# Kernel tuning notes

Measured on AMD Instinct MI355X. Metric: run time of the kernel, lower is better.

The kernel has to match this reference:

```python
import jax, jax.numpy as jnp
import numpy as np

NEG_SLOPE = 0.2


def gat_layer(x, src, dst, W, a_src, a_dst, b, heads, out_c, concat):
    N = x.shape[0]
    h = (x @ W).reshape(N, heads, out_c)                      # [N,H,C]
    alpha_s = jnp.einsum('nhc,hc->nh', h, a_src)              # [N,H]
    alpha_d = jnp.einsum('nhc,hc->nh', h, a_dst)              # [N,H]
    e = jax.nn.leaky_relu(alpha_s[src] + alpha_d[dst], NEG_SLOPE)  # [E,H]
    # softmax over incoming edges per destination node (segment softmax)
    m = jax.ops.segment_max(e, dst, num_segments=N)
    m = jnp.where(jnp.isfinite(m), m, 0.0)
    ex = jnp.exp(e - m[dst])
    denom = jax.ops.segment_sum(ex, dst, num_segments=N)
    alpha = ex / (denom[dst] + 1e-16)                         # [E,H]
    out = jax.ops.segment_sum(alpha[:, :, None] * h[src], dst, num_segments=N)  # [N,H,C]
    out = out.reshape(N, heads * out_c) if concat else out.mean(axis=1)
    return out + b


def setup_inputs() -> dict:
    key = jax.random.key(0)
    ks = jax.random.split(key, 12)
    N, E, D, H, C, G = 20000, 160000, 256, 4, 128, 64
    x = jax.random.normal(ks[0], (N, D), dtype=jnp.float32)
    edge_index = jax.random.randint(ks[1], (2, E), 0, N)
    batch = jnp.sort(jax.random.randint(ks[2], (N,), 0, G))
    s = 0.05
    params = {
        'W1': jax.random.normal(ks[3], (D, H * C), jnp.float32) * s,
        'a_src1': jax.random.normal(ks[4], (H, C), jnp.float32) * s,
        'a_dst1': jax.random.normal(ks[5], (H, C), jnp.float32) * s,
        'b1': jnp.zeros((H * C,), jnp.float32),
        'W2': jax.random.normal(ks[6], (H * C, C), jnp.float32) * s,
        'a_src2': jax.random.normal(ks[7], (1, C), jnp.float32) * s,
        'a_dst2': jax.random.normal(ks[8], (1, C), jnp.float32) * s,
        'b2': jnp.zeros((C,), jnp.float32),
        'fc1_W': jax.random.normal(ks[9], (C, C // 2), jnp.float32) * s,
        'fc1_b': jnp.zeros((C // 2,), jnp.float32),
        'fc2_W': jax.random.normal(ks[10], (C // 2, 1), jnp.float32) * s,
        'fc2_b': jnp.zeros((1,), jnp.float32),
    }
    return dict(x=x, edge_index=edge_index, batch=batch, **params)


def reference(x, edge_index, batch, W1, a_src1, a_dst1, b1, W2, a_src2, a_dst2, b2,
              fc1_W, fc1_b, fc2_W, fc2_b):
    N = x.shape[0]
    G = 64  # number of graphs
    # add self-loops (PyG GATConv default)
    loop = jnp.arange(N, dtype=edge_index.dtype)
    src = jnp.concatenate([edge_index[0], loop])
    dst = jnp.concatenate([edge_index[1], loop])
    h = jax.nn.relu(gat_layer(x, src, dst, W1, a_src1, a_dst1, b1, 4, 128, True))
    h = gat_layer(h, src, dst, W2, a_src2, a_dst2, b2, 1, 128, False)
    # global mean pool per graph
    sums = jax.ops.segment_sum(h, batch, num_segments=G)
    cnts = jax.ops.segment_sum(jnp.ones((N,), h.dtype), batch, num_segments=G)
    pooled = sums / jnp.maximum(cnts, 1.0)[:, None]          # [G,128]
    out = jax.nn.relu(pooled @ fc1_W + fc1_b)
    return out @ fc2_W + fc2_b                                # [G,1]
```

## Files before the change

### kernel.cpp

```cpp
#include <hip/hip_runtime.h>
#include <hip/hip_bf16.h>
#include <cstdint>
#include <cstddef>

#define NEG_SLOPE 0.2f

typedef __attribute__((ext_vector_type(8))) __bf16 bf16x8;
typedef __attribute__((ext_vector_type(4))) __bf16 bf16x4;
typedef __attribute__((ext_vector_type(2))) __bf16 bf16x2;
typedef __attribute__((ext_vector_type(4))) float  f32x4;

__device__ __forceinline__ float lrelu(float v) {
    return (v < 0.f) ? NEG_SLOPE * v : v;
}

__device__ __forceinline__ unsigned fkey(float x) {
    unsigned b = __float_as_uint(x);
    return b ^ (unsigned)(((int)b >> 31) | 0x80000000);
}
__device__ __forceinline__ float funkey(unsigned k) {
    unsigned b = (k & 0x80000000u) ? (k ^ 0x80000000u) : ~k;
    return __uint_as_float(b);
}

__global__ __launch_bounds__(256) void gemm2_sum(
    const __bf16* __restrict__ A,
    const __bf16* __restrict__ Bt,
    __bf16* __restrict__ Cout,
    const float* __restrict__ ps_part, const float* __restrict__ pd_part,
    float* __restrict__ as2, float* __restrict__ ad2,
    unsigned* __restrict__ gmax2u,
    int M, int MB)
{
    if ((int)blockIdx.y >= MB) {
        int chunk = ((int)blockIdx.y - MB) * 2 + (int)blockIdx.x;
        int i = chunk * 256 + threadIdx.x;
        float lm = -1e30f;
        if (i < M) {
            float4 p = *(const float4*)&ps_part[(size_t)i * 4];
            float4 q = *(const float4*)&pd_part[(size_t)i * 4];
            float s = (p.x + p.y) + (p.z + p.w);
            float d = (q.x + q.y) + (q.z + q.w);
            as2[i] = s;
            ad2[i] = d;
            lm = s;
        }
        #pragma unroll
        for (int t = 1; t < 64; t <<= 1) lm = fmaxf(lm, __shfl_xor(lm, t));
        if ((threadIdx.x & 63) == 0) atomicMax(gmax2u, fkey(lm));
        return;
    }

    const int tid  = threadIdx.x;
    const int wave = tid >> 6, lane = tid & 63;
    const int wr = wave >> 1, wc = wave & 1;
    const int rowbase = blockIdx.y * 64 + wr * 32;
    const int colbase = blockIdx.x * 64 + wc * 32;
    const int l15 = lane & 15, kg = lane >> 4;
    const int K = 512, N = 128;

    size_t aoff[2], boff[2];
    #pragma unroll
    for (int mf = 0; mf < 2; ++mf) {
        int r = rowbase + mf * 16 + l15;
        if (r > M - 1) r = M - 1;
        aoff[mf] = (size_t)r * K + kg * 8;
    }
    #pragma unroll
    for (int nf = 0; nf < 2; ++nf) {
        int c = colbase + nf * 16 + l15;
        boff[nf] = (size_t)c * K + kg * 8;
    }

    f32x4 acc[2][2];
    #pragma unroll
    for (int mf = 0; mf < 2; ++mf)
        #pragma unroll
        for (int nf = 0; nf < 2; ++nf)
            acc[mf][nf] = (f32x4){0.f, 0.f, 0.f, 0.f};

    #pragma unroll 2
    for (int k0 = 0; k0 < K; k0 += 32) {
        bf16x8 af[2], bfr[2];
        #pragma unroll
        for (int mf = 0; mf < 2; ++mf)
            af[mf] = *(const bf16x8*)(A + aoff[mf] + k0);
        #pragma unroll
        for (int nf = 0; nf < 2; ++nf)
            bfr[nf] = *(const bf16x8*)(Bt + boff[nf] + k0);
        #pragma unroll
        for (int mf = 0; mf < 2; ++mf)
            #pragma unroll
            for (int nf = 0; nf < 2; ++nf)
                acc[mf][nf] = __builtin_amdgcn_mfma_f32_16x16x32_bf16(af[mf], bfr[nf], acc[mf][nf], 0, 0, 0);
    }

    #pragma unroll
    for (int mf = 0; mf < 2; ++mf)
        #pragma unroll
        for (int j = 0; j < 4; ++j) {
            int r = rowbase + mf * 16 + kg * 4 + j;
            if (r < M) {
                #pragma unroll
                for (int nf = 0; nf < 2; ++nf) {
                    int c = colbase + nf * 16 + l15;
                    Cout[(size_t)r * N + c] = (__bf16)acc[mf][nf][j];
                }
            }
        }
}

__global__ __launch_bounds__(256) void gemm1_agg(
    const __bf16* __restrict__ aggx,
    const __bf16* __restrict__ w1t,
    const float* __restrict__ b1, const float* __restrict__ wsd2,
    __bf16* __restrict__ out1b,
    float* __restrict__ ps_part, float* __restrict__ pd_part,
    int M)
{
    const int head = blockIdx.x;
    const int tid  = threadIdx.x;
    const int wave = tid >> 6, lane = tid & 63;
    const int wr = wave >> 1, wc = wave & 1;
    const int rowbase = blockIdx.y * 128 + wr * 64;
    const int l15 = lane & 15, kg = lane >> 4;

    size_t aoff[4], boff[4];
    #pragma unroll
    for (int mf = 0; mf < 4; ++mf) {
        int r = rowbase + mf * 16 + l15;
        if (r > M - 1) r = M - 1;
        aoff[mf] = (size_t)r * 1024 + head * 256 + kg * 8;
    }
    #pragma unroll
    for (int nf = 0; nf < 4; ++nf) {
        int c = head * 128 + wc * 64 + nf * 16 + l15;
        boff[nf] = (size_t)c * 256 + kg * 8;
    }

    f32x4 acc[4][4];
    #pragma unroll
    for (int mf = 0; mf < 4; ++mf)
        #pragma unroll
        for (int nf = 0; nf < 4; ++nf)
            acc[mf][nf] = (f32x4){0.f, 0.f, 0.f, 0.f};

    #pragma unroll 2
    for (int k0 = 0; k0 < 256; k0 += 32) {
        bf16x8 af[4], bfr[4];
        #pragma unroll
        for (int mf = 0; mf < 4; ++mf)
            af[mf] = *(const bf16x8*)(aggx + aoff[mf] + k0);
        #pragma unroll
        for (int nf = 0; nf < 4; ++nf)
            bfr[nf] = *(const bf16x8*)(w1t + boff[nf] + k0);
        #pragma unroll
        for (int mf = 0; mf < 4; ++mf)
            #pragma unroll
            for (int nf = 0; nf < 4; ++nf)
                acc[mf][nf] = __builtin_amdgcn_mfma_f32_16x16x32_bf16(af[mf], bfr[nf], acc[mf][nf], 0, 0, 0);
    }

    __shared__ float smp[2][128], smd[2][128];

    #pragma unroll
    for (int mf = 0; mf < 4; ++mf)
        #pragma unroll
        for (int j = 0; j < 4; ++j) {
            int r = rowbase + mf * 16 + kg * 4 + j;
            float ps = 0.f, pd = 0.f;
            #pragma unroll
            for (int nf = 0; nf < 4; ++nf) {
                int col = head * 128 + wc * 64 + nf * 16 + l15;
                float o = fmaxf(acc[mf][nf][j] + b1[col], 0.f);
                if (r < M)
                    out1b[(size_t)r * 512 + col] = (__bf16)o;
                ps = fmaf(o, wsd2[col], ps);
                pd = fmaf(o, wsd2[512 + col], pd);
            }
            #pragma unroll
            for (int t = 1; t < 16; t <<= 1) {
                ps += __shfl_xor(ps, t);
                pd += __shfl_xor(pd, t);
            }
            if (l15 == 0) {
                int lr = wr * 64 + mf * 16 + kg * 4 + j;
                smp[wc][lr] = ps;
                smd[wc][lr] = pd;
            }
        }
    __syncthreads();
    if (tid < 128) {
        int r = blockIdx.y * 128 + tid;
        if (r < M) {
            ps_part[(size_t)r * 4 + head] = smp[0][tid] + smp[1][tid];
            pd_part[(size_t)r * 4 + head] = smd[0][tid] + smd[1][tid];
        }
    }
}

__global__ void prep_kernel(const float* __restrict__ W1, const float* __restrict__ W2,
                            const float* __restrict__ as1w, const float* __restrict__ ad1w,
                            const float* __restrict__ as2w, const float* __restrict__ ad2w,
                            const int* __restrict__ batch,
                            __bf16* __restrict__ w1t, __bf16* __restrict__ w2t,
                            float* __restrict__ wsd1, float* __restrict__ wsd2,
                            int* __restrict__ gstart, int* __restrict__ cnt,
                            unsigned* __restrict__ gmax2u,
                            int N, int G)
{
    int t = blockIdx.x * 256 + threadIdx.x;
    if (t < 131072) {
        int i = t;
        int k = i >> 9, n = i & 511;
        w1t[n * 256 + k] = (__bf16)W1[i];
    } else if (t < 196608) {
        int j = t - 131072;
        int k = j >> 7, n = j & 127;
        w2t[n * 512 + k] = (__bf16)W2[j];
    } else if (t < 199680) {
        int t2 = t - 196608;
        if (t2 < 2048) {
            int k = t2 >> 3, v = t2 & 7, h = v >> 1;
            const float* av = (v & 1) ? (ad1w + h * 128) : (as1w + h * 128);
            float s = 0.f;
            for (int c = 0; c < 128; ++c) s += W1[k * 512 + h * 128 + c] * av[c];
            wsd1[v * 256 + k] = s;
        } else {
            int t3 = t2 - 2048;
            int k = t3 >> 1, v = t3 & 1;
            const float* av = v ? ad2w : as2w;
            float s = 0.f;
            for (int c = 0; c < 128; ++c) s += W2[k * 128 + c] * av[c];
            wsd2[v * 512 + k] = s;
        }
    } else if (t < 199680 + N) {
        int n = t - 199680;
        int b    = batch[n];
        int prev = (n == 0) ? -1 : batch[n - 1];
        for (int g = prev + 1; g <= b; ++g) gstart[g] = n;
        if (n == N - 1) {
            for (int g = b + 1; g <= G; ++g) gstart[g] = N;
        }
    } else if (t < 199680 + 2 * N) {
        cnt[t - 199680 - N] = 0;
    } else if (t == 199680 + 2 * N) {
        *gmax2u = fkey(-1e30f);
    }
}

__global__ __launch_bounds__(256) void count_cvtx(
    const int* __restrict__ ei, int* __restrict__ cnt,
    const float* __restrict__ x, const float* __restrict__ wsd1,
    __bf16* __restrict__ xb, float* __restrict__ as1_, float* __restrict__ ad1_,
    int ET, int E0, int N, int CB)
{
    if ((int)blockIdx.x < CB) {
        int base = (blockIdx.x * 256 + threadIdx.x) * 2;
        #pragma unroll
        for (int k = 0; k < 2; ++k) {
            int e = base + k;
            if (e < ET) {
                int d = (e < E0) ? ei[E0 + e] : (e - E0);
                atomicAdd(&cnt[d], 1);
            }
        }
        return;
    }
    int bid = blockIdx.x - CB;
    int wave = threadIdx.x >> 6, lane = threadIdx.x & 63;
    int n = bid * 4 + wave;
    if (n >= N) return;
    float4 xv = *(const float4*)&x[(size_t)n * 256 + lane * 4];
    bf16x4 xo;
    xo[0] = (__bf16)xv.x; xo[1] = (__bf16)xv.y; xo[2] = (__bf16)xv.z; xo[3] = (__bf16)xv.w;
    *(bf16x4*)&xb[(size_t)n * 256 + lane * 4] = xo;
    float p[8];
    #pragma unroll
    for (int v = 0; v < 8; ++v) {
        float4 wv = *(const float4*)&wsd1[v * 256 + lane * 4];
        p[v] = xv.x * wv.x + xv.y * wv.y + xv.z * wv.z + xv.w * wv.w;
    }
    #pragma unroll
    for (int v = 0; v < 8; ++v)
        #pragma unroll
        for (int s = 1; s < 64; s <<= 1) p[v] += __shfl_xor(p[v], s);
    if (lane == 0) {
        #pragma unroll
        for (int h = 0; h < 4; ++h) {
            as1_[n * 4 + h] = p[2 * h];
            ad1_[n * 4 + h] = p[2 * h + 1];
        }
    }
}

__global__ __launch_bounds__(1024) void scan_gmax(
    const int* __restrict__ cnt, int* __restrict__ offs, int* __restrict__ cur,
    const float* __restrict__ as1_, float* __restrict__ gmax1, int n)
{
    constexpr int CHUNK = 20;
    int t = threadIdx.x;
    int base = t * CHUNK;
    int v[CHUNK];
    int s = 0;
    #pragma unroll
    for (int i = 0; i < CHUNK; ++i) {
        int idx = base + i;
        int xv = (idx < n) ? cnt[idx] : 0;
        v[i] = s; s += xv;
    }
    int lane = t & 63, w = t >> 6;
    int sc = s;
    #pragma unroll
    for (int d = 1; d < 64; d <<= 1) {
        int o = __shfl_up(sc, d);
        if (lane >= d) sc += o;
    }
    __shared__ int wt[16], wb[17];
    __shared__ float gsm[16][4];
    if (lane == 63) wt[w] = sc;
    __syncthreads();
    if (t == 0) {
        int acc = 0;
        for (int i = 0; i < 16; ++i) { wb[i] = acc; acc += wt[i]; }
        wb[16] = acc;
    }
    __syncthreads();
    int ebase = wb[w] + (sc - s);
    #pragma unroll
    for (int i = 0; i < CHUNK; ++i) {
        int idx = base + i;
        if (idx < n) {
            int o = ebase + v[i];
            offs[idx] = o;
            cur[idx]  = o;
        }
    }
    if (t == 0) offs[n] = wb[16];

    float lm0 = -1e30f, lm1 = -1e30f, lm2 = -1e30f, lm3 = -1e30f;
    for (int i = t; i < n; i += 1024) {
        float4 a = *(const float4*)&as1_[(size_t)i * 4];
        lm0 = fmaxf(lm0, a.x); lm1 = fmaxf(lm1, a.y);
        lm2 = fmaxf(lm2, a.z); lm3 = fmaxf(lm3, a.w);
    }
    #pragma unroll
    for (int d = 1; d < 64; d <<= 1) {
        lm0 = fmaxf(lm0, __shfl_xor(lm0, d));
        lm1 = fmaxf(lm1, __shfl_xor(lm1, d));
        lm2 = fmaxf(lm2, __shfl_xor(lm2, d));
        lm3 = fmaxf(lm3, __shfl_xor(lm3, d));
    }
    if (lane == 0) {
        gsm[w][0] = lm0; gsm[w][1] = lm1; gsm[w][2] = lm2; gsm[w][3] = lm3;
    }
    __syncthreads();
    if (t == 0) {
        float m0 = -1e30f, m1 = -1e30f, m2 = -1e30f, m3 = -1e30f;
        for (int i = 0; i < 16; ++i) {
            m0 = fmaxf(m0, gsm[i][0]); m1 = fmaxf(m1, gsm[i][1]);
            m2 = fmaxf(m2, gsm[i][2]); m3 = fmaxf(m3, gsm[i][3]);
        }
        gmax1[0] = m0; gmax1[1] = m1; gmax1[2] = m2; gmax1[3] = m3;
    }
}

__global__ void scatter_kernel(const int* __restrict__ ei, int* __restrict__ cur,
                               int* __restrict__ srcs, int ET, int E0)
{
    int e = blockIdx.x * blockDim.x + threadIdx.x;
    if (e >= ET) return;
    int d = (e < E0) ? ei[E0 + e] : (e - E0);
    int s = (e < E0) ? ei[e] : (e - E0);
    int pos = atomicAdd(&cur[d], 1);
    srcs[pos] = s;
}

__global__ __launch_bounds__(256) void aggx_kernel(
    const __bf16* __restrict__ xb, const int* __restrict__ offs,
    const int* __restrict__ srcs,
    const float* __restrict__ as1_, const float* __restrict__ ad1_,
    const float* __restrict__ gmax1,
    __bf16* __restrict__ aggx, int N)
{
    __shared__ float w4s[4][64][4];
    __shared__ int   sidx[4][64];
    int wave = threadIdx.x >> 6, lane = threadIdx.x & 63;
    int n = blockIdx.x * 4 + wave;
    if (n >= N) return;
    int s0 = offs[n], s1 = offs[n + 1];
    float4 adv = *(const float4*)&ad1_[(size_t)n * 4];
    float m0 = lrelu(gmax1[0] + adv.x);
    float m1 = lrelu(gmax1[1] + adv.y);
    float m2 = lrelu(gmax1[2] + adv.z);
    float m3 = lrelu(gmax1[3] + adv.w);

    float d0 = 0.f, d1 = 0.f, d2 = 0.f, d3 = 0.f;
    float a0[4] = {0.f,0.f,0.f,0.f}, a1[4] = {0.f,0.f,0.f,0.f};
    float a2[4] = {0.f,0.f,0.f,0.f}, a3[4] = {0.f,0.f,0.f,0.f};
    const __bf16* xbase = xb + lane * 4;

    for (int base = s0; base < s1; base += 64) {
        int cnt = min(64, s1 - base);
        if (lane < cnt) {
            int s = srcs[base + lane];
            float4 av = *(const float4*)&as1_[(size_t)s * 4];
            float w0 = __expf(lrelu(av.x + adv.x) - m0);
            float w1 = __expf(lrelu(av.y + adv.y) - m1);
            float w2 = __expf(lrelu(av.z + adv.z) - m2);
            float w3 = __expf(lrelu(av.w + adv.w) - m3);
            d0 += w0; d1 += w1; d2 += w2; d3 += w3;
            sidx[wave][lane] = s;
            w4s[wave][lane][0] = w0; w4s[wave][lane][1] = w1;
            w4s[wave][lane][2] = w2; w4s[wave][lane][3] = w3;
        }
        int j = 0;
        for (; j + 7 < cnt; j += 8) {
            int s_[8]; float4 w_[8]; bf16x4 xv_[8];
            #pragma unroll
            for (int i = 0; i < 8; ++i) {
                s_[i] = sidx[wave][j + i];
                w_[i] = *(const float4*)&w4s[wave][j + i][0];
            }
            #pragma unroll
            for (int i = 0; i < 8; ++i)
                xv_[i] = *(const bf16x4*)(xbase + (size_t)s_[i] * 256);
            #pragma unroll
            for (int i = 0; i < 8; ++i) {
                float xf[4];
                #pragma unroll
                for (int c = 0; c < 4; ++c) xf[c] = (float)xv_[i][c];
                #pragma unroll
                for (int c = 0; c < 4; ++c) {
                    a0[c] = fmaf(w_[i].x, xf[c], a0[c]);
                    a1[c] = fmaf(w_[i].y, xf[c], a1[c]);
                    a2[c] = fmaf(w_[i].z, xf[c], a2[c]);
                    a3[c] = fmaf(w_[i].w, xf[c], a3[c]);
                }
            }
        }
        for (; j < cnt; ++j) {
            int s = sidx[wave][j];
            float4 w = *(const float4*)&w4s[wave][j][0];
            bf16x4 xv = *(const bf16x4*)(xbase + (size_t)s * 256);
            float xf[4];
            #pragma unroll
            for (int c = 0; c < 4; ++c) xf[c] = (float)xv[c];
            #pragma unroll
            for (int c = 0; c < 4; ++c) {
                a0[c] = fmaf(w.x, xf[c], a0[c]);
                a1[c] = fmaf(w.y, xf[c], a1[c]);
                a2[c] = fmaf(w.z, xf[c], a2[c]);
                a3[c] = fmaf(w.w, xf[c], a3[c]);
            }
        }
    }

    #pragma unroll
    for (int t = 1; t < 64; t <<= 1) {
        d0 += __shfl_xor(d0, t);
        d1 += __shfl_xor(d1, t);
        d2 += __shfl_xor(d2, t);
        d3 += __shfl_xor(d3, t);
    }

    float i0 = 1.f / (d0 + 1e-16f);
    float i1 = 1.f / (d1 + 1e-16f);
    float i2 = 1.f / (d2 + 1e-16f);
    float i3 = 1.f / (d3 + 1e-16f);
    __bf16* obase = aggx + (size_t)n * 1024 + lane * 4;
    bf16x4 o;
    #pragma unroll
    for (int c = 0; c < 4; ++c) o[c] = (__bf16)(a0[c] * i0);
    *(bf16x4*)(obase + 0)   = o;
    #pragma unroll
    for (int c = 0; c < 4; ++c) o[c] = (__bf16)(a1[c] * i1);
    *(bf16x4*)(obase + 256) = o;
    #pragma unroll
    for (int c = 0; c < 4; ++c) o[c] = (__bf16)(a2[c] * i2);
    *(bf16x4*)(obase + 512) = o;
    #pragma unroll
    for (int c = 0; c < 4; ++c) o[c] = (__bf16)(a3[c] * i3);
    *(bf16x4*)(obase + 768) = o;
}

__global__ __launch_bounds__(256) void aggregate2_kernel(
    const __bf16* __restrict__ h2b, const int* __restrict__ offs,
    const int* __restrict__ srcs,
    const float* __restrict__ as2, const float* __restrict__ ad2,
    const unsigned* __restrict__ gmax2u,
    const float* __restrict__ b2, float* __restrict__ out2, int N)
{
    __shared__ float wls[4][64];
    __shared__ int   sidx[4][64];
    int wave = threadIdx.x >> 6, lane = threadIdx.x & 63;
    int n = blockIdx.x * 4 + wave;
    if (n >= N) return;
    int s0 = offs[n], s1 = offs[n + 1];
    float adn = ad2[n];
    float m = lrelu(funkey(*gmax2u) + adn);

    float den = 0.f;
    float c0 = 0.f, c1 = 0.f;
    const __bf16* hbase = h2b + lane * 2;

    for (int base = s0; base < s1; base += 64) {
        int cnt = min(64, s1 - base);
        if (lane < cnt) {
            int s = srcs[base + lane];
            float w = __expf(lrelu(as2[s] + adn) - m);
            den += w;
            sidx[wave][lane] = s;
            wls[wave][lane]  = w;
        }
        int j = 0;
        for (; j + 7 < cnt; j += 8) {
            int s_[8]; float w_[8]; bf16x2 h_[8];
            #pragma unroll
            for (int i = 0; i < 8; ++i) {
                s_[i] = sidx[wave][j + i];
                w_[i] = wls[wave][j + i];
            }
            #pragma unroll
            for (int i = 0; i < 8; ++i)
                h_[i] = *(const bf16x2*)(hbase + (size_t)s_[i] * 128);
            #pragma unroll
            for (int i = 0; i < 8; ++i) {
                c0 = fmaf(w_[i], (float)h_[i][0], c0);
                c1 = fmaf(w_[i], (float)h_[i][1], c1);
            }
        }
        for (; j < cnt; ++j) {
            int s = sidx[wave][j];
            float w = wls[wave][j];
            bf16x2 hv = *(const bf16x2*)(hbase + (size_t)s * 128);
            c0 = fmaf(w, (float)hv[0], c0);
            c1 = fmaf(w, (float)hv[1], c1);
        }
    }

    #pragma unroll
    for (int t = 1; t < 64; t <<= 1) den += __shfl_xor(den, t);
    float inv = 1.f / (den + 1e-16f);
    float2 o;
    o.x = c0 * inv + b2[lane * 2 + 0];
    o.y = c1 * inv + b2[lane * 2 + 1];
    *(float2*)&out2[(size_t)n * 128 + lane * 2] = o;
}

#define POOL_S 16
__global__ void pool_stage1(const float* __restrict__ out2, const int* __restrict__ gstart,
                            float* __restrict__ partial, int C)
{
    int g = blockIdx.x, slice = blockIdx.y;
    int c = threadIdx.x;
    int s = gstart[g], e = gstart[g + 1];
    int len = e - s;
    int chunk = (len + POOL_S - 1) / POOL_S;
    int n0 = s + slice * chunk;
    int n1 = min(n0 + chunk, e);
    float acc = 0.f;
    for (int n = n0; n < n1; ++n) acc += out2[(size_t)n * C + c];
    partial[((size_t)g * POOL_S + slice) * C + c] = acc;
}

__global__ __launch_bounds__(128) void pool_head(
    const float* __restrict__ partial, const int* __restrict__ gstart,
    const float* __restrict__ fc1W, const float* __restrict__ fc1b,
    const float* __restrict__ fc2W, const float* __restrict__ fc2b,
    float* __restrict__ out)
{
    int g = blockIdx.x;
    int t = threadIdx.x;
    __shared__ float pl[128];
    float acc = 0.f;
    #pragma unroll
    for (int s = 0; s < POOL_S; ++s)
        acc += partial[((size_t)g * POOL_S + s) * 128 + t];
    float cntf = (float)(gstart[g + 1] - gstart[g]);
    pl[t] = acc / fmaxf(cntf, 1.0f);
    __syncthreads();
    if (t < 64) {
        float v = 0.f;
        for (int c = 0; c < 128; ++c)
            v += pl[c] * fc1W[c * 64 + t];
        v = fmaxf(v + fc1b[t], 0.f) * fc2W[t];
        #pragma unroll
        for (int s = 32; s > 0; s >>= 1) v += __shfl_down(v, s);
        if (t == 0) out[g] = v + fc2b[0];
    }
}

extern "C" void kernel_launch(void* const* d_in, const int* in_sizes, int n_in,
                              void* d_out, int out_size, void* d_ws, size_t ws_size,
                              hipStream_t stream)
{
    const float* x    = (const float*)d_in[0];
    const int*   ei   = (const int*)d_in[1];
    const int*   batch= (const int*)d_in[2];
    const float* W1   = (const float*)d_in[3];
    const float* as1w = (const float*)d_in[4];
    const float* ad1w = (const float*)d_in[5];
    const float* b1   = (const float*)d_in[6];
    const float* W2   = (const float*)d_in[7];
    const float* as2w = (const float*)d_in[8];
    const float* ad2w = (const float*)d_in[9];
    const float* b2   = (const float*)d_in[10];
    const float* fc1W = (const float*)d_in[11];
    const float* fc1b = (const float*)d_in[12];
    const float* fc2W = (const float*)d_in[13];
    const float* fc2b = (const float*)d_in[14];
    float* out = (float*)d_out;

    const int D = 256, C = 128, G = 64;
    const int N  = in_sizes[0] / D;
    const int E0 = in_sizes[1] / 2;
    const int ET = E0 + N;

    char* p = (char*)d_ws;
    auto alloc = [&](size_t bytes) -> char* {
        char* r = p;
        p += (bytes + 255) & ~(size_t)255;
        return r;
    };
    __bf16* xb    = (__bf16*)alloc((size_t)N * D * 2);
    __bf16* aggx  = (__bf16*)alloc((size_t)N * 4 * 256 * 2);
    __bf16* out1b = (__bf16*)alloc((size_t)N * 512 * 2);
    __bf16* h2b   = (__bf16*)alloc((size_t)N * C * 2);
    float*  out2  = (float*)alloc((size_t)N * C * 4);
    __bf16* w1t   = (__bf16*)alloc((size_t)256 * 512 * 2);
    __bf16* w2t   = (__bf16*)alloc((size_t)512 * 128 * 2);
    float* wsd1   = (float*)alloc(8 * 256 * 4);
    float* wsd2   = (float*)alloc(2 * 512 * 4);
    float* gmax1  = (float*)alloc(4 * 4);
    unsigned* gmax2u = (unsigned*)alloc(4);
    float* as1_   = (float*)alloc((size_t)N * 4 * 4);
    float* ad1_   = (float*)alloc((size_t)N * 4 * 4);
    float* ps_part= (float*)alloc((size_t)N * 4 * 4);
    float* pd_part= (float*)alloc((size_t)N * 4 * 4);
    float* as2    = (float*)alloc((size_t)N * 4);
    float* ad2    = (float*)alloc((size_t)N * 4);
    int*   cnt    = (int*)alloc((size_t)N * 4);
    int*   cur    = (int*)alloc((size_t)N * 4);
    int*   offs   = (int*)alloc((size_t)(N + 1) * 4);
    int*   srcs   = (int*)alloc((size_t)ET * 4);
    int*   gstart = (int*)alloc((size_t)(G + 1) * 4);
    float* partial= (float*)alloc((size_t)G * POOL_S * C * 4);

    {
        int total = 199680 + 2 * N + 1;
        prep_kernel<<<(total + 255) / 256, 256, 0, stream>>>(
            W1, W2, as1w, ad1w, as2w, ad2w, batch,
            w1t, w2t, wsd1, wsd2, gstart, cnt, gmax2u, N, G);
    }

    {
        int CB = (ET + 511) / 512;
        count_cvtx<<<CB + N / 4, 256, 0, stream>>>(
            ei, cnt, x, wsd1, xb, as1_, ad1_, ET, E0, N, CB);
    }

    scan_gmax<<<1, 1024, 0, stream>>>(cnt, offs, cur, as1_, gmax1, N);

    scatter_kernel<<<(ET + 255) / 256, 256, 0, stream>>>(ei, cur, srcs, ET, E0);

    aggx_kernel<<<(N + 3) / 4, 256, 0, stream>>>(
        xb, offs, srcs, as1_, ad1_, gmax1, aggx, N);

    gemm1_agg<<<dim3(4, (N + 127) / 128), 256, 0, stream>>>(
        aggx, w1t, b1, wsd2, out1b, ps_part, pd_part, N);

    {
        int MB = (N + 63) / 64;
        int SB = ((N + 255) / 256 + 1) / 2;
        gemm2_sum<<<dim3(2, MB + SB), 256, 0, stream>>>(
            out1b, w2t, h2b, ps_part, pd_part, as2, ad2, gmax2u, N, MB);
    }

    aggregate2_kernel<<<(N + 3) / 4, 256, 0, stream>>>(
        h2b, offs, srcs, as2, ad2, gmax2u, b2, out2, N);

    pool_stage1<<<dim3(G, POOL_S), C, 0, stream>>>(out2, gstart, partial, C);
    pool_head<<<G, 128, 0, stream>>>(partial, gstart, fc1W, fc1b, fc2W, fc2b, out);
}
```

Before: 195.4 us.

## Stage gemm1 A tile in LDS and shrink row tile to 64

The layer-1 aggregated-feature GEMM now copies a 64x256 A tile per head into padded shared memory, and the four waves read their fragments from there rather than each pulling them from global memory. The block tile goes from 128 rows to 64 rows with each wave covering 32 columns, which doubles the grid size and cuts accumulator registers. The aim is fewer redundant global loads and better occupancy. The cost is about 34KB of LDS per block, an extra barrier, and B weights being fetched from global once per 64 rows instead of once per 128.

```diff
diff --git a/kernel.cpp b/kernel.cpp
--- a/kernel.cpp
+++ b/kernel.cpp
@@ -118,60 +118,67 @@
     float* __restrict__ ps_part, float* __restrict__ pd_part,
     int M)
 {
+    __shared__ __bf16 As[64][264];
+    __shared__ float smp[4][64], smd[4][64];
+
     const int head = blockIdx.x;
+    const int rowtile = blockIdx.y * 64;
     const int tid  = threadIdx.x;
     const int wave = tid >> 6, lane = tid & 63;
-    const int wr = wave >> 1, wc = wave & 1;
-    const int rowbase = blockIdx.y * 128 + wr * 64;
     const int l15 = lane & 15, kg = lane >> 4;
 
-    size_t aoff[4], boff[4];
-    #pragma unroll
-    for (int mf = 0; mf < 4; ++mf) {
-        int r = rowbase + mf * 16 + l15;
-        if (r > M - 1) r = M - 1;
-        aoff[mf] = (size_t)r * 1024 + head * 256 + kg * 8;
-    }
-    #pragma unroll
-    for (int nf = 0; nf < 4; ++nf) {
-        int c = head * 128 + wc * 64 + nf * 16 + l15;
+    #pragma unroll
+    for (int it = 0; it < 8; ++it) {
+        int flat  = it * 256 + tid;
+        int row   = flat >> 5;
+        int chunk = flat & 31;
+        int gr = rowtile + row;
+        if (gr > M - 1) gr = M - 1;
+        bf16x8 v = *(const bf16x8*)(aggx + (size_t)gr * 1024 + head * 256 + chunk * 8);
+        *(bf16x8*)&As[row][chunk * 8] = v;
+    }
+    __syncthreads();
+
+    size_t boff[2];
+    #pragma unroll
+    for (int nf = 0; nf < 2; ++nf) {
+        int c = head * 128 + wave * 32 + nf * 16 + l15;
         boff[nf] = (size_t)c * 256 + kg * 8;
     }
 
-    f32x4 acc[4][4];
+    f32x4 acc[4][2];
     #pragma unroll
     for (int mf = 0; mf < 4; ++mf)
         #pragma unroll
-        for (int nf = 0; nf < 4; ++nf)
+        for (int nf = 0; nf < 2; ++nf)
             acc[mf][nf] = (f32x4){0.f, 0.f, 0.f, 0.f};
 
     #pragma unroll 2
     for (int k0 = 0; k0 < 256; k0 += 32) {
-        bf16x8 af[4], bfr[4];
+        bf16x8 af[4], bfr[2];
         #pragma unroll
         for (int mf = 0; mf < 4; ++mf)
-            af[mf] = *(const bf16x8*)(aggx + aoff[mf] + k0);
-        #pragma unroll
-        for (int nf = 0; nf < 4; ++nf)
+            af[mf] = *(const bf16x8*)&As[mf * 16 + l15][k0 + kg * 8];
+        #pragma unroll
+        for (int nf = 0; nf < 2; ++nf)
             bfr[nf] = *(const bf16x8*)(w1t + boff[nf] + k0);
         #pragma unroll
         for (int mf = 0; mf < 4; ++mf)
             #pragma unroll
-            for (int nf = 0; nf < 4; ++nf)
+            for (int nf = 0; nf < 2; ++nf)
                 acc[mf][nf] = __builtin_amdgcn_mfma_f32_16x16x32_bf16(af[mf], bfr[nf], acc[mf][nf], 0, 0, 0);
     }
 
-    __shared__ float smp[2][128], smd[2][128];
-
     #pragma unroll
     for (int mf = 0; mf < 4; ++mf)
         #pragma unroll
         for (int j = 0; j < 4; ++j) {
-            int r = rowbase + mf * 16 + kg * 4 + j;
+            int lr = mf * 16 + kg * 4 + j;
+            int r  = rowtile + lr;
             float ps = 0.f, pd = 0.f;
             #pragma unroll
-            for (int nf = 0; nf < 4; ++nf) {
-                int col = head * 128 + wc * 64 + nf * 16 + l15;
+            for (int nf = 0; nf < 2; ++nf) {
+                int col = head * 128 + wave * 32 + nf * 16 + l15;
                 float o = fmaxf(acc[mf][nf][j] + b1[col], 0.f);
                 if (r < M)
                     out1b[(size_t)r * 512 + col] = (__bf16)o;
@@ -184,17 +191,16 @@
                 pd += __shfl_xor(pd, t);
             }
             if (l15 == 0) {
-                int lr = wr * 64 + mf * 16 + kg * 4 + j;
-                smp[wc][lr] = ps;
-                smd[wc][lr] = pd;
+                smp[wave][lr] = ps;
+                smd[wave][lr] = pd;
             }
         }
     __syncthreads();
-    if (tid < 128) {
-        int r = blockIdx.y * 128 + tid;
+    if (tid < 64) {
+        int r = rowtile + tid;
         if (r < M) {
-            ps_part[(size_t)r * 4 + head] = smp[0][tid] + smp[1][tid];
-            pd_part[(size_t)r * 4 + head] = smd[0][tid] + smd[1][tid];
+            ps_part[(size_t)r * 4 + head] = (smp[0][tid] + smp[1][tid]) + (smp[2][tid] + smp[3][tid]);
+            pd_part[(size_t)r * 4 + head] = (smd[0][tid] + smd[1][tid]) + (smd[2][tid] + smd[3][tid]);
         }
     }
 }
@@ -667,7 +673,7 @@
     aggx_kernel<<<(N + 3) / 4, 256, 0, stream>>>(
         xb, offs, srcs, as1_, ad1_, gmax1, aggx, N);
 
-    gemm1_agg<<<dim3(4, (N + 127) / 128), 256, 0, stream>>>(
+    gemm1_agg<<<dim3(4, (N + 63) / 64), 256, 0, stream>>>(
         aggx, w1t, b1, wsd2, out1b, ps_part, pd_part, N);
 
     {
```

Result: faster. 185.0 us (median of 2 runs) (-5.3%).
